# Performance work log

Measured on AMD Instinct MI355X. Metric: run time of the kernel, lower is better.

The kernel has to match this reference:

```python
import jax, jax.numpy as jnp
import numpy as np

B, N, K, A = 2, 4096, 20, 12
DIMS = [32, 64, 128, 256, 512]
POOL_RATE, POOL_K = 4, 4


def knn_index(v, k):
    # v: (b, n, 3) -> (b, n, k) nearest neighbors, self excluded
    d2 = jnp.sum(v * v, axis=-1)
    dist = d2[:, :, None] + d2[:, None, :] - 2.0 * jnp.einsum('bnd,bmd->bnm', v, v)
    _, idx = jax.lax.top_k(-dist, k + 1)
    return idx[:, :, 1:]


def gather_pos(v, idx):
    return jax.vmap(lambda vv, ii: vv[ii])(v, idx)  # (b, n, k, 3)


def gather_fea(fm, idx):
    return jax.vmap(lambda f, ii: f[:, ii, :])(fm, idx)  # (b, c, n, k, a)


def nbr_dirs(v, idx):
    d = gather_pos(v, idx) - v[:, :, None, :]
    return d / (jnp.linalg.norm(d, axis=-1, keepdims=True) + 1e-8)


def conv_surface(idx, v, K0):
    # K0: (C0, A, 3) learned direction kernels; output (b, C0, n, A)
    d = nbr_dirs(v, idx)  # (b,n,k,3)
    theta = jax.nn.relu(jnp.einsum('bnkd,cad->bnkca', d, K0))
    return jnp.transpose(jnp.max(theta, axis=2), (0, 2, 1, 3))


def equi_conv(idx, v, fm, dirs, Wc, bc, Ws):
    # fm: (b, cin, n, a) -> (b, cout, n, a)
    d = nbr_dirs(v, idx)
    theta = jax.nn.relu(jnp.einsum('bnkd,ad->bnka', d, dirs))  # (b,n,k,a)
    fn = gather_fea(fm, idx)  # (b,cin,n,k,a)
    fs = jnp.einsum('bcnka,co->bonka', fn, Ws) * theta[:, None]
    fs = jnp.max(fs, axis=3)  # max over neighbors -> (b,cout,n,a)
    fc = jnp.einsum('bcna,co->bona', fm, Wc) + bc[None, :, None, None]
    return fc + fs


def batchnorm(x, g, b):
    m = jnp.mean(x, axis=(0, 2, 3), keepdims=True)
    var = jnp.var(x, axis=(0, 2, 3), keepdims=True)
    return (x - m) * jax.lax.rsqrt(var + 1e-5) * g[None, :, None, None] + b[None, :, None, None]


def pool(v, fm):
    idx = knn_index(v, POOL_K)
    fn = jnp.max(gather_fea(fm, idx), axis=3)
    fm_p = jnp.maximum(fm, fn)
    sel = jnp.arange(0, v.shape[1], POOL_RATE)  # strided subsample
    return v[:, sel], fm_p[:, :, sel]


def fea_of(fm):
    return jnp.transpose(jnp.max(fm, axis=-1), (0, 2, 1))  # (b,n,c)


def setup_inputs() -> dict:
    key = jax.random.key(0)
    ks = iter(jax.random.split(key, 32))
    p = {'vertices': jax.random.normal(next(ks), (B, N, 3), jnp.float32)}
    p['K0'] = jax.random.normal(next(ks), (DIMS[0], A, 3), jnp.float32) * 0.1
    for i, (ci, co) in enumerate(zip(DIMS[:4], DIMS[1:]), start=1):
        s = 1.0 / np.sqrt(ci).astype(np.float32)
        p[f'dirs{i}'] = jax.random.normal(next(ks), (A, 3), jnp.float32) * 0.1
        p[f'Wc{i}'] = jax.random.normal(next(ks), (ci, co), jnp.float32) * s
        p[f'bc{i}'] = jnp.zeros((co,), jnp.float32)
        p[f'Ws{i}'] = jax.random.normal(next(ks), (ci, co), jnp.float32) * s
    for i, c in enumerate([DIMS[1], DIMS[2], DIMS[3]], start=1):
        p[f'g{i}'] = jnp.ones((c,), jnp.float32)
        p[f'b{i}'] = jnp.zeros((c,), jnp.float32)
    return p


def reference(vertices, K0, dirs1, Wc1, bc1, Ws1, dirs2, Wc2, bc2, Ws2,
              dirs3, Wc3, bc3, Ws3, dirs4, Wc4, bc4, Ws4,
              g1, b1, g2, b2, g3, b3):
    idx = knn_index(vertices, K)
    fm0 = jax.nn.relu(conv_surface(idx, vertices, K0))
    fm1 = jax.nn.relu(batchnorm(equi_conv(idx, vertices, fm0, dirs1, Wc1, bc1, Ws1), g1, b1))
    v1, fmp1 = pool(vertices, fm1)
    idx1 = knn_index(v1, min(K, v1.shape[1] // 8))
    fm2 = jax.nn.relu(batchnorm(equi_conv(idx1, v1, fmp1, dirs2, Wc2, bc2, Ws2), g2, b2))
    fm3 = jax.nn.relu(batchnorm(equi_conv(idx1, v1, fm2, dirs3, Wc3, bc3, Ws3), g3, b3))
    v2, fmp2 = pool(v1, fm3)
    idx2 = knn_index(v2, min(K, v2.shape[1] // 8))
    fm4 = equi_conv(idx2, v2, fmp2, dirs4, Wc4, bc4, Ws4)
    return fea_of(fm0), fea_of(fm1), fea_of(fm2), fea_of(fm3), fea_of(fm4)
```

## Files before the change

kernel.cpp:

```cpp
#include <hip/hip_runtime.h>
#include <hip/hip_bf16.h>
#include <math.h>

typedef unsigned short u16;
typedef unsigned long long u64;
#define DEV static __device__ __forceinline__

constexpr int Bz = 2, N0 = 4096, N1 = 1024, N2 = 256, KNN = 20, NA = 12;
constexpr int C0 = 32, C1 = 64, C2 = 128, C3 = 256, C4 = 512;
constexpr int BNG = 32;

constexpr size_t OFF_V0F   = 0;
constexpr size_t OFF_V1F   = 32768;
constexpr size_t OFF_V2F   = 40960;
constexpr size_t OFF_K0F   = 43008;
constexpr size_t OFF_DIRS  = 44160;
constexpr size_t OFF_WC    = 44304;
constexpr size_t OFF_WS    = 218384;
constexpr size_t OFF_BC    = 392464;
constexpr size_t OFF_BN    = 393424;
constexpr size_t OFF_FLAG  = 394832;
constexpr size_t OFF_IDX0  = 394848;
constexpr size_t OFF_IDX1  = 558688;
constexpr size_t OFF_IDX2  = 599648;
constexpr size_t OFF_PART  = 609888;
constexpr size_t PART_SZ   = 28672;
constexpr size_t OFF_HALF  = OFF_PART + PART_SZ;

constexpr size_t HA = 0;
constexpr size_t HB = 3145728;
constexpr size_t HG = 9437184;
constexpr size_t HP = HG + 3145728;

constexpr size_t OUT0 = 0;
constexpr size_t OUT1 = OUT0 + (size_t)Bz*N0*C0;
constexpr size_t OUT2 = OUT1 + (size_t)Bz*N0*C1;
constexpr size_t OUT3 = OUT2 + (size_t)Bz*N1*C2;
constexpr size_t OUT4 = OUT3 + (size_t)Bz*N1*C3;

DEV float b2f(u16 v) { return __uint_as_float(((unsigned int)v) << 16); }
DEV u16 f2b(float f) {
  unsigned int u = __float_as_uint(f);
  unsigned int lsb = (u >> 16) & 1u;
  return (u16)((u + 0x7fffu + lsb) >> 16);
}
DEV unsigned packb(float a, float b) {
  return (unsigned)f2b(a) | ((unsigned)f2b(b) << 16);
}

DEV u64 shflx64(u64 v, int m) {
  int lo = __shfl_xor((int)(unsigned)v, m, 64);
  int hi = __shfl_xor((int)(unsigned)(v >> 32), m, 64);
  return ((u64)(unsigned)hi << 32) | (unsigned)lo;
}
DEV int mbcnt64(u64 m) {
  return __builtin_amdgcn_mbcnt_hi((unsigned)(m >> 32),
         __builtin_amdgcn_mbcnt_lo((unsigned)m, 0));
}

DEV void st12(float* dst, const float* v) {
  float4 a{v[0],v[1],v[2],v[3]}, b{v[4],v[5],v[6],v[7]}, c{v[8],v[9],v[10],v[11]};
  ((float4*)dst)[0] = a; ((float4*)dst)[1] = b; ((float4*)dst)[2] = c;
}
DEV void st12(u16* dst, const float* v) {
  uint2 a{packb(v[0],v[1]), packb(v[2],v[3])};
  uint2 b{packb(v[4],v[5]), packb(v[6],v[7])};
  uint2 c{packb(v[8],v[9]), packb(v[10],v[11])};
  ((uint2*)dst)[0] = a; ((uint2*)dst)[1] = b; ((uint2*)dst)[2] = c;
}

struct InPtrs { const void* p[24]; };

__global__ void eq_convert_all(InPtrs in, float* ws) {
  __shared__ int sflag;
  {
    const u16* v = (const u16*)in.p[0];
    if (threadIdx.x < 64) {
      int bad = 0;
      #pragma unroll
      for (int j = 0; j < 4; ++j) {
        unsigned u = v[threadIdx.x*4 + j];
        int ex = (u >> 7) & 0xFF;
        bad += (((u & 0x7FFFu) != 0u) && (ex < 64 || ex > 191)) ? 1 : 0;
      }
      int tot = bad;
      #pragma unroll
      for (int s = 32; s > 0; s >>= 1) tot += __shfl_xor(tot, s, 64);
      if (threadIdx.x == 0) sflag = (tot >= 8) ? 1 : 0;
    }
    __syncthreads();
  }
  int f32mode = sflag;
  int t = blockIdx.x * blockDim.x + threadIdx.x;
  if (t < Bz*N0) {
    float x, y, z;
    if (f32mode) { const float* v = (const float*)in.p[0]; x=v[t*3]; y=v[t*3+1]; z=v[t*3+2]; }
    else { const u16* v = (const u16*)in.p[0]; x=b2f(v[t*3]); y=b2f(v[t*3+1]); z=b2f(v[t*3+2]); }
    float4 o; o.x=x; o.y=y; o.z=z; o.w=(x*x + y*y) + z*z;
    ((float4*)(ws + OFF_V0F))[t] = o;
    int b = t / N0, i = t % N0;
    if ((i & 3) == 0)  ((float4*)(ws + OFF_V1F))[b*N1 + (i >> 2)] = o;
    if ((i & 15) == 0) ((float4*)(ws + OFF_V2F))[b*N2 + (i >> 4)] = o;
    return;
  }
  int r = t - Bz*N0;
  if (r >= 351312) {
    int z = r - 351312;
    if (z < (int)PART_SZ) ws[OFF_PART + z] = 0.f;
    return;
  }
  const int cnt[23] = {1152, 36,2048,64,2048, 36,8192,128,8192,
                       36,32768,256,32768, 36,131072,512,131072,
                       64,64,128,128,256,256};
  const size_t off[23] = {OFF_K0F,
    OFF_DIRS+0,   OFF_WC+0,     OFF_BC+0,   OFF_WS+0,
    OFF_DIRS+36,  OFF_WC+2048,  OFF_BC+64,  OFF_WS+2048,
    OFF_DIRS+72,  OFF_WC+10240, OFF_BC+192, OFF_WS+10240,
    OFF_DIRS+108, OFF_WC+43008, OFF_BC+448, OFF_WS+43008,
    OFF_BN+0, OFF_BN+64, OFF_BN+128, OFF_BN+256, OFF_BN+384, OFF_BN+640};
  for (int i = 0; i < 23; ++i) {
    if (r < cnt[i]) {
      float val = f32mode ? ((const float*)in.p[i+1])[r] : b2f(((const u16*)in.p[i+1])[r]);
      ws[off[i] + r] = val;
      return;
    }
    r -= cnt[i];
  }
}

DEV unsigned umin(unsigned a, unsigned b) { return a < b ? a : b; }
DEV unsigned umax(unsigned a, unsigned b) { return a > b ? a : b; }

DEV unsigned cand_ud(const float4 vq, const float4 vc) {
  float dt = fmaf(vq.x, vc.x, fmaf(vq.y, vc.y, vq.z*vc.z));
  float d  = fmaf(-2.0f, dt, vq.w + vc.w);
  unsigned u = __float_as_uint(d);
  return u ^ ((unsigned)(((int)u) >> 31) | 0x80000000u);
}

template<int NPTS>
DEV void knn_body(int blk, const float4* __restrict__ vf, int* __restrict__ idx_out,
                  char* smem) {
  constexpr int CPL = NPTS/64;
  u64* selw_base = (u64*)smem;
  int* extr_base = (int*)(smem + 4*64*8);
  int wave = threadIdx.x >> 6, lane = threadIdx.x & 63;
  u64* selw = selw_base + wave*64;
  int* extrw = extr_base + wave*24;
  int qid = blk*4 + wave;
  int b = qid / NPTS, q = qid % NPTS;
  const float4* vb = vf + (size_t)b*NPTS;
  float4 vq = vb[q];

  unsigned k1=~0u, k2=~0u, k3=~0u, k4=~0u;
  #pragma unroll 8
  for (int j = 0; j < CPL; ++j) {
    float4 vc = vb[j*64 + lane];
    unsigned key = cand_ud(vq, vc);
    unsigned nk1 = umin(key, k1);
    unsigned nk2 = umin(umax(key, k1), k2);
    unsigned nk3 = umin(umax(key, k2), k3);
    unsigned nk4 = umin(umax(key, k3), k4);
    k1 = nk1; k2 = nk2; k3 = nk3; k4 = nk4;
  }

  unsigned p = 0;
  for (int bit = 31; bit >= 0; --bit) {
    unsigned T = p | (1u << bit);
    u64 m1 = __ballot(k1 < T), m2 = __ballot(k2 < T);
    u64 m3 = __ballot(k3 < T), m4 = __ballot(k4 < T);
    int cnt = __popcll(m1) + __popcll(m2) + __popcll(m3) + __popcll(m4);
    if (cnt < KNN+1) p = T;
  }
  size_t obase = (size_t)qid*KNN;
  bool need_fb = (CPL > 4) && (__ballot(k4 <= p) != 0ULL);

  if (!need_fb) {
    int base = 0;
    #pragma unroll 4
    for (int j = 0; j < CPL; ++j) {
      float4 vc = vb[j*64 + lane];
      unsigned ud = cand_ud(vq, vc);
      bool sel = (ud <= p);
      u64 m = __ballot(sel);
      int pos = base + mbcnt64(m);
      if (sel && pos < 64)
        selw[pos] = ((u64)ud << 32) | (unsigned)(j*64 + lane);
      base += __popcll(m);
    }
    int S = (base < 64) ? base : 64;
    if (lane < S) {
      u64 mykey = selw[lane];
      int rank = 0;
      for (int j = 0; j < S; ++j) rank += (selw[j] < mykey) ? 1 : 0;
      if (rank >= 1 && rank <= KNN)
        idx_out[obase + rank - 1] = (int)(unsigned)(mykey & 0xFFFFFFFFu);
    }
  } else {
    const u64 KINF = ~0ULL;
    u64 K1=KINF, K2=KINF, K3=KINF, K4=KINF;
    for (int j = 0; j < CPL; ++j) {
      int c = j*64 + lane;
      u64 k = ((u64)cand_ud(vq, vb[c]) << 32) | (unsigned)c;
      bool lt1 = k < K1, lt2 = k < K2, lt3 = k < K3, lt4 = k < K4;
      K4 = lt3 ? K3 : (lt4 ? k : K4);
      K3 = lt2 ? K2 : (lt3 ? k : K3);
      K2 = lt1 ? K1 : (lt2 ? k : K2);
      K1 = lt1 ? k  : K1;
    }
    for (int r = 0; r < KNN+1; ++r) {
      u64 g = K1;
      #pragma unroll
      for (int s = 32; s; s >>= 1) { u64 o = shflx64(g, s); g = (o < g) ? o : g; }
      int gidx = (int)(unsigned)(g & 0xFFFFFFFFu);
      if (lane == 0) {
        extrw[r] = gidx;
        if (r > 0) idx_out[obase + r - 1] = gidx;
      }
      if (r < KNN && lane == (gidx & 63)) {
        K1 = K2; K2 = K3; K3 = K4; K4 = KINF;
        if (K1 == KINF) {
          for (int j = 0; j < CPL; ++j) {
            int c = j*64 + lane;
            u64 k = ((u64)cand_ud(vq, vb[c]) << 32) | (unsigned)c;
            bool ex = false;
            for (int e = 0; e <= r; ++e) ex |= (extrw[e] == c);
            if (!ex) {
              bool lt1 = k < K1, lt2 = k < K2, lt3 = k < K3, lt4 = k < K4;
              K4 = lt3 ? K3 : (lt4 ? k : K4);
              K3 = lt2 ? K2 : (lt3 ? k : K3);
              K2 = lt1 ? K1 : (lt2 ? k : K2);
              K1 = lt1 ? k  : K1;
            }
          }
        }
      }
    }
  }
}

__global__ __launch_bounds__(256) void eq_knn_all(
    const float4* __restrict__ v0, int* __restrict__ i0,
    const float4* __restrict__ v1, int* __restrict__ i1,
    const float4* __restrict__ v2, int* __restrict__ i2) {
  __shared__ __align__(16) char smem[4*64*8 + 4*24*4];
  int blk = blockIdx.x;
  constexpr int NB0 = Bz*N0/4, NB1 = Bz*N1/4;
  if (blk < NB0)            knn_body<N0>(blk, v0, i0, smem);
  else if (blk < NB0+NB1)   knn_body<N1>(blk - NB0, v1, i1, smem);
  else                      knn_body<N2>(blk - NB0 - NB1, v2, i2, smem);
}

__global__ __launch_bounds__(128) void eq_conv_surface(
    const float4* __restrict__ v0f, const int* __restrict__ idx0,
    const float* __restrict__ K0f, u16* __restrict__ fm0, float* __restrict__ out0) {
  int bq = blockIdx.x;
  int b = bq >> 12;
  __shared__ float dk[KNN][3];
  __shared__ float row[C0*NA];
  int tid = threadIdx.x;
  if (tid < KNN) {
    int m = idx0[(size_t)bq*KNN + tid];
    float4 vq = v0f[bq];
    float4 vm = v0f[(size_t)b*N0 + m];
    float dx = vm.x - vq.x, dy = vm.y - vq.y, dz = vm.z - vq.z;
    float nrm = sqrtf((dx*dx + dy*dy) + dz*dz) + 1e-8f;
    dk[tid][0] = dx/nrm; dk[tid][1] = dy/nrm; dk[tid][2] = dz/nrm;
  }
  __syncthreads();
  for (int t4 = tid; t4 < C0*NA/4; t4 += 128) {
    const float* kd = K0f + (size_t)t4*12;
    float4 k0 = *(const float4*)(kd);
    float4 k1 = *(const float4*)(kd + 4);
    float4 k2 = *(const float4*)(kd + 8);
    float m0=0.f, m1=0.f, m2=0.f, m3=0.f;
    #pragma unroll
    for (int k = 0; k < KNN; ++k) {
      float dx = dk[k][0], dy = dk[k][1], dz = dk[k][2];
      m0 = fmaxf(m0, (dx*k0.x + dy*k0.y) + dz*k0.z);
      m1 = fmaxf(m1, (dx*k0.w + dy*k1.x) + dz*k1.y);
      m2 = fmaxf(m2, (dx*k1.z + dy*k1.w) + dz*k2.x);
      m3 = fmaxf(m3, (dx*k2.y + dy*k2.z) + dz*k2.w);
    }
    uint2 r; r.x = packb(m0, m1); r.y = packb(m2, m3);
    ((uint2*)fm0)[(size_t)bq*(C0*NA/4) + t4] = r;
    row[4*t4+0] = m0; row[4*t4+1] = m1; row[4*t4+2] = m2; row[4*t4+3] = m3;
  }
  __syncthreads();
  if (tid < C0) {
    float m = row[tid*NA];
    #pragma unroll
    for (int a = 1; a < NA; ++a) m = fmaxf(m, row[tid*NA + a]);
    out0[(size_t)bq*C0 + tid] = m;
  }
}

template<int CI, int CO, typename TO>
__global__ __launch_bounds__(256) void eq_linear4(
    const u16* __restrict__ in, const float* __restrict__ Wc,
    const float* __restrict__ Ws, const float* __restrict__ bias,
    TO* __restrict__ fc, u16* __restrict__ g) {
  constexpr int PPB = 512 / CO;
  constexpr int RS = CI*NA + 4;
  __shared__ float lds[PPB*RS];
  int tid = threadIdx.x;
  int mat = blockIdx.x & 1;
  int pt0 = (blockIdx.x >> 1) * PPB;
  constexpr int E = PPB*CI*NA;
  for (int t = tid; t < E; t += 256) {
    int pt = t / (CI*NA), r = t % (CI*NA);
    lds[pt*RS + r] = b2f(in[((size_t)(pt0+pt))*CI*NA + r]);
  }
  __syncthreads();
  constexpr int TPP = CO/2;
  int opair = tid % TPP, pt = tid / TPP;
  int o0 = opair*2;
  const float* W = mat ? Ws : Wc;
  const float* row = lds + pt*RS;
  float a0[NA], a1[NA];
  #pragma unroll
  for (int a = 0; a < NA; ++a) { a0[a]=0.f; a1[a]=0.f; }
  #pragma unroll 4
  for (int c = 0; c < CI; ++c) {
    float2 w2 = *(const float2*)(W + (size_t)c*CO + o0);
    float4 i0 = *(const float4*)(row + c*NA);
    float4 i1 = *(const float4*)(row + c*NA + 4);
    float4 i2 = *(const float4*)(row + c*NA + 8);
    float iv[NA] = {i0.x,i0.y,i0.z,i0.w, i1.x,i1.y,i1.z,i1.w, i2.x,i2.y,i2.z,i2.w};
    #pragma unroll
    for (int a = 0; a < NA; ++a) {
      a0[a] += iv[a]*w2.x; a1[a] += iv[a]*w2.y;
    }
  }
  size_t ptg = pt0 + pt;
  if (mat == 0) {
    float b0 = bias[o0], b1 = bias[o0+1];
    #pragma unroll
    for (int a = 0; a < NA; ++a) { a0[a] += b0; a1[a] += b1; }
    st12(fc + ((size_t)ptg*CO + o0)*NA, a0);
    st12(fc + ((size_t)ptg*CO + o0 + 1)*NA, a1);
  } else {
    st12(g + ((size_t)ptg*CO + o0)*NA, a0);
    st12(g + ((size_t)ptg*CO + o0 + 1)*NA, a1);
  }
}

__global__ __launch_bounds__(256) void eq_fsmax(
    const u16* __restrict__ g, const float4* __restrict__ vf,
    const float* __restrict__ dirs, const int* __restrict__ idx,
    u16* __restrict__ out, float* __restrict__ part, int npts, int co) {
  int bq = blockIdx.x;
  int b = bq / npts;
  __shared__ float th[KNN*NA];
  __shared__ float dk[KNN][3];
  __shared__ int nb[KNN];
  __shared__ float sstat[2][C3];
  int tid = threadIdx.x;
  if (tid < KNN) {
    int m = idx[(size_t)bq*KNN + tid];
    nb[tid] = m;
    float4 vq = vf[bq];
    float4 vm = vf[(size_t)b*npts + m];
    float dx = vm.x - vq.x, dy = vm.y - vq.y, dz = vm.z - vq.z;
    float nrm = sqrtf((dx*dx + dy*dy) + dz*dz) + 1e-8f;
    dk[tid][0] = dx/nrm; dk[tid][1] = dy/nrm; dk[tid][2] = dz/nrm;
  }
  sstat[0][tid] = 0.f; sstat[1][tid] = 0.f;
  __syncthreads();
  if (tid < KNN*NA) {
    int k = tid / NA, a = tid % NA;
    float s = (dk[k][0]*dirs[a*3] + dk[k][1]*dirs[a*3+1]) + dk[k][2]*dirs[a*3+2];
    th[tid] = fmaxf(s, 0.f);
  }
  __syncthreads();
  int quarter = co*NA/4;
  uint2* dst = (uint2*)(out + (size_t)bq*co*NA);
  const uint2* gb = (const uint2*)(g + (size_t)b*npts*co*NA);
  for (int t4 = tid; t4 < quarter; t4 += 256) {
    int a = (4*t4) % NA;
    const float* tha = th + a;
    float m0=-3.0e38f, m1=-3.0e38f, m2=-3.0e38f, m3=-3.0e38f;
    #pragma unroll 5
    for (int k = 0; k < KNN; ++k) {
      uint2 pv = gb[(size_t)nb[k]*quarter + t4];
      float4 tv = *(const float4*)(tha + k*NA);
      m0 = fmaxf(m0, tv.x*b2f((u16)(pv.x)));
      m1 = fmaxf(m1, tv.y*b2f((u16)(pv.x >> 16)));
      m2 = fmaxf(m2, tv.z*b2f((u16)(pv.y)));
      m3 = fmaxf(m3, tv.w*b2f((u16)(pv.y >> 16)));
    }
    uint2 d = dst[t4];
    float v0 = b2f((u16)d.x) + m0;
    float v1 = b2f((u16)(d.x >> 16)) + m1;
    float v2 = b2f((u16)d.y) + m2;
    float v3 = b2f((u16)(d.y >> 16)) + m3;
    uint2 r; r.x = packb(v0, v1); r.y = packb(v2, v3);
    dst[t4] = r;
    int ch = t4 / 3;
    atomicAdd(&sstat[0][ch], (v0 + v1) + (v2 + v3));
    atomicAdd(&sstat[1][ch], (v0*v0 + v1*v1) + (v2*v2 + v3*v3));
  }
  __syncthreads();
  if (tid < co) {
    float* pg = part + (size_t)(bq & (BNG-1))*2*co;
    atomicAdd(&pg[tid], sstat[0][tid]);
    atomicAdd(&pg[co + tid], sstat[1][tid]);
  }
}

template<int SPL>
__global__ __launch_bounds__(256) void eq_fsmax_fea(
    const u16* __restrict__ g, const float* __restrict__ fcin,
    const float4* __restrict__ vf, const float* __restrict__ dirs,
    const int* __restrict__ idx, float* __restrict__ outfea,
    int npts, int co) {
  constexpr int CHUNK = C4 / SPL;
  int part = blockIdx.x % SPL;
  int bq = blockIdx.x / SPL;
  int b = bq / npts;
  __shared__ float th[KNN*NA];
  __shared__ float dk[KNN][3];
  __shared__ int nb[KNN];
  __shared__ float row[CHUNK*NA];
  int tid = threadIdx.x;
  if (tid < KNN) {
    int m = idx[(size_t)bq*KNN + tid];
    nb[tid] = m;
    float4 vq = vf[bq];
    float4 vm = vf[(size_t)b*npts + m];
    float dx = vm.x - vq.x, dy = vm.y - vq.y, dz = vm.z - vq.z;
    float nrm = sqrtf((dx*dx + dy*dy) + dz*dz) + 1e-8f;
    dk[tid][0] = dx/nrm; dk[tid][1] = dy/nrm; dk[tid][2] = dz/nrm;
  }
  __syncthreads();
  if (tid < KNN*NA) {
    int k = tid / NA, a = tid % NA;
    float s = (dk[k][0]*dirs[a*3] + dk[k][1]*dirs[a*3+1]) + dk[k][2]*dirs[a*3+2];
    th[tid] = fmaxf(s, 0.f);
  }
  __syncthreads();
  int o0 = part * CHUNK;
  const float4* fcr = (const float4*)(fcin + ((size_t)bq*co + o0)*NA);
  const uint2* gb = (const uint2*)(g + (size_t)b*npts*co*NA + (size_t)o0*NA);
  int gquarter = co*NA/4;
  for (int t4 = tid; t4 < CHUNK*NA/4; t4 += 256) {
    int a = (4*t4) % NA;
    const float* tha = th + a;
    float m0=-3.0e38f, m1=-3.0e38f, m2=-3.0e38f, m3=-3.0e38f;
    #pragma unroll 5
    for (int k = 0; k < KNN; ++k) {
      uint2 pv = gb[(size_t)nb[k]*gquarter + t4];
      float4 tv = *(const float4*)(tha + k*NA);
      m0 = fmaxf(m0, tv.x*b2f((u16)(pv.x)));
      m1 = fmaxf(m1, tv.y*b2f((u16)(pv.x >> 16)));
      m2 = fmaxf(m2, tv.z*b2f((u16)(pv.y)));
      m3 = fmaxf(m3, tv.w*b2f((u16)(pv.y >> 16)));
    }
    float4 fc4 = fcr[t4];
    row[4*t4+0] = fc4.x + m0;
    row[4*t4+1] = fc4.y + m1;
    row[4*t4+2] = fc4.z + m2;
    row[4*t4+3] = fc4.w + m3;
  }
  __syncthreads();
  for (int o = tid; o < CHUNK; o += 256) {
    float m = row[o*NA];
    #pragma unroll
    for (int a = 1; a < NA; ++a) m = fmaxf(m, row[o*NA + a]);
    outfea[(size_t)bq*co + o0 + o] = m;
  }
}

__global__ __launch_bounds__(256) void eq_bnrelu_fea(
    u16* __restrict__ fm, const float* __restrict__ part,
    const float* __restrict__ gamma, const float* __restrict__ beta,
    float* __restrict__ outfea, int npts, int co) {
  int bq = blockIdx.x;
  int tid = threadIdx.x;
  __shared__ float sc[C3], sh[C3];
  __shared__ float row[C3*NA];
  for (int o = tid; o < co; o += 256) {
    float s = 0.f, s2 = 0.f;
    for (int g = 0; g < BNG; ++g) {
      s  += part[(size_t)g*2*co + o];
      s2 += part[(size_t)g*2*co + co + o];
    }
    float cnt = (float)(Bz*npts*NA);
    float mean = s / cnt;
    float var = fmaxf(s2 / cnt - mean*mean, 0.f);
    float inv = 1.0f / sqrtf(var + 1e-5f);
    sc[o] = gamma[o] * inv;
    sh[o] = beta[o] - mean * gamma[o] * inv;
  }
  __syncthreads();
  uint2* p = (uint2*)(fm + (size_t)bq*co*NA);
  int quarter = co*NA/4;
  for (int t4 = tid; t4 < quarter; t4 += 256) {
    int o = (4*t4) / NA;
    float s = sc[o], h = sh[o];
    uint2 pv = p[t4];
    float v0 = fmaxf(b2f((u16)pv.x)*s + h, 0.f);
    float v1 = fmaxf(b2f((u16)(pv.x >> 16))*s + h, 0.f);
    float v2 = fmaxf(b2f((u16)pv.y)*s + h, 0.f);
    float v3 = fmaxf(b2f((u16)(pv.y >> 16))*s + h, 0.f);
    uint2 r; r.x = packb(v0, v1); r.y = packb(v2, v3);
    p[t4] = r;
    row[4*t4+0] = v0; row[4*t4+1] = v1; row[4*t4+2] = v2; row[4*t4+3] = v3;
  }
  __syncthreads();
  for (int o = tid; o < co; o += 256) {
    float m = row[o*NA];
    #pragma unroll
    for (int a = 1; a < NA; ++a) m = fmaxf(m, row[o*NA + a]);
    outfea[(size_t)bq*co + o] = m;
  }
}

__global__ __launch_bounds__(256) void eq_pool(
    const u16* __restrict__ fm, const int* __restrict__ idx,
    u16* __restrict__ fmp, int npts, int c) {
  int ns = npts / 4;
  int bj = blockIdx.x;
  int b = bj / ns, j = bj % ns;
  int q = 4*j;
  size_t bq = (size_t)b*npts + q;
  __shared__ int nb[4];
  if (threadIdx.x < 4) nb[threadIdx.x] = idx[bq*KNN + threadIdx.x];
  __syncthreads();
  int quarter = c*NA/4;
  const uint2* base = (const uint2*)(fm + (size_t)b*npts*c*NA);
  const uint2* p0 = base + (size_t)q*quarter;
  uint2* dst = (uint2*)(fmp + (size_t)bj*c*NA);
  for (int t4 = threadIdx.x; t4 < quarter; t4 += 256) {
    uint2 v = p0[t4];
    float m0 = b2f((u16)v.x), m1 = b2f((u16)(v.x >> 16));
    float m2 = b2f((u16)v.y), m3 = b2f((u16)(v.y >> 16));
    #pragma unroll
    for (int kk = 0; kk < 4; ++kk) {
      uint2 w = base[(size_t)nb[kk]*quarter + t4];
      m0 = fmaxf(m0, b2f((u16)w.x));
      m1 = fmaxf(m1, b2f((u16)(w.x >> 16)));
      m2 = fmaxf(m2, b2f((u16)w.y));
      m3 = fmaxf(m3, b2f((u16)(w.y >> 16)));
    }
    uint2 r; r.x = packb(m0, m1); r.y = packb(m2, m3);
    dst[t4] = r;
  }
}

extern "C" void kernel_launch(void* const* d_in, const int* in_sizes, int n_in,
                              void* d_out, int out_size, void* d_ws, size_t ws_size,
                              hipStream_t stream) {
  float* ws = (float*)d_ws;
  float* out = (float*)d_out;
  u16* arena = (u16*)(ws + OFF_HALF);

  InPtrs ip;
  for (int i = 0; i < 24; ++i) ip.p[i] = d_in[i];

  float4* v0f = (float4*)(ws + OFF_V0F);
  float4* v1f = (float4*)(ws + OFF_V1F);
  float4* v2f = (float4*)(ws + OFF_V2F);
  int* idx0 = (int*)(ws + OFF_IDX0);
  int* idx1 = (int*)(ws + OFF_IDX1);
  int* idx2 = (int*)(ws + OFF_IDX2);
  u16* bufA = arena + HA;
  u16* bufB = arena + HB;
  float* fc4f = (float*)(arena + HB);
  u16* bufG = arena + HG;
  u16* bufP = arena + HP;
  float* partA = ws + OFF_PART;
  float* partB = ws + OFF_PART + 4096;
  float* partC = ws + OFF_PART + 12288;
  const float* DIRS = ws + OFF_DIRS;

  {
    int total = Bz*N0 + 351312 + (int)PART_SZ;
    eq_convert_all<<<(total + 255)/256, 256, 0, stream>>>(ip, ws);
  }

  eq_knn_all<<<Bz*N0/4 + Bz*N1/4 + Bz*N2/4, 256, 0, stream>>>(v0f, idx0, v1f, idx1, v2f, idx2);
  eq_conv_surface<<<Bz*N0, 128, 0, stream>>>(v0f, idx0, ws + OFF_K0F, bufA, out + OUT0);

  eq_linear4<C0, C1, u16><<<(Bz*N0/8)*2, 256, 0, stream>>>(bufA, ws + OFF_WC + 0, ws + OFF_WS + 0,
                                                           ws + OFF_BC + 0, bufB, bufG);
  eq_fsmax<<<Bz*N0, 256, 0, stream>>>(bufG, v0f, DIRS + 0, idx0, bufB, partA, N0, C1);
  eq_bnrelu_fea<<<Bz*N0, 256, 0, stream>>>(bufB, partA, ws + OFF_BN + 0, ws + OFF_BN + 64,
                                           out + OUT1, N0, C1);

  eq_pool<<<Bz*N1, 256, 0, stream>>>(bufB, idx0, bufP, N0, C1);

  eq_linear4<C1, C2, u16><<<(Bz*N1/4)*2, 256, 0, stream>>>(bufP, ws + OFF_WC + 2048, ws + OFF_WS + 2048,
                                                           ws + OFF_BC + 64, bufA, bufG);
  eq_fsmax<<<Bz*N1, 256, 0, stream>>>(bufG, v1f, DIRS + 36, idx1, bufA, partB, N1, C2);
  eq_bnrelu_fea<<<Bz*N1, 256, 0, stream>>>(bufA, partB, ws + OFF_BN + 128, ws + OFF_BN + 256,
                                           out + OUT2, N1, C2);

  eq_linear4<C2, C3, u16><<<(Bz*N1/2)*2, 256, 0, stream>>>(bufA, ws + OFF_WC + 10240, ws + OFF_WS + 10240,
                                                           ws + OFF_BC + 192, bufB, bufG);
  eq_fsmax<<<Bz*N1, 256, 0, stream>>>(bufG, v1f, DIRS + 72, idx1, bufB, partC, N1, C3);
  eq_bnrelu_fea<<<Bz*N1, 256, 0, stream>>>(bufB, partC, ws + OFF_BN + 384, ws + OFF_BN + 640,
                                           out + OUT3, N1, C3);

  eq_pool<<<Bz*N2, 256, 0, stream>>>(bufB, idx1, bufP, N1, C3);

  eq_linear4<C3, C4, float><<<(Bz*N2)*2, 256, 0, stream>>>(bufP, ws + OFF_WC + 43008, ws + OFF_WS + 43008,
                                                           ws + OFF_BC + 448, fc4f, bufG);
  eq_fsmax_fea<4><<<Bz*N2*4, 256, 0, stream>>>(bufG, fc4f, v2f, DIRS + 108, idx2, out + OUT4, N2, C4);
}
```

Baseline: 499.6 us.

## Process four KNN queries per wave and keep candidate indices in registers

Each wavefront now handles four query points at once, so every candidate point load is reused across four distance computations. The per-lane top-4 lists now carry indices alongside distances, which removes the second pass over all candidates to collect the selected ones. The fallback path is seeded from the register lists. In exchange, register pressure grows considerably, the grid has four times fewer blocks, and the threshold search runs four times per wave.

```diff
diff --git a/kernel.cpp b/kernel.cpp
--- a/kernel.cpp
+++ b/kernel.cpp
@@ -128,9 +128,6 @@
   }
 }
 
-DEV unsigned umin(unsigned a, unsigned b) { return a < b ? a : b; }
-DEV unsigned umax(unsigned a, unsigned b) { return a > b ? a : b; }
-
 DEV unsigned cand_ud(const float4 vq, const float4 vc) {
   float dt = fmaf(vq.x, vc.x, fmaf(vq.y, vc.y, vq.z*vc.z));
   float d  = fmaf(-2.0f, dt, vq.w + vc.w);
@@ -139,98 +136,116 @@
 }
 
 template<int NPTS>
-DEV void knn_body(int blk, const float4* __restrict__ vf, int* __restrict__ idx_out,
-                  char* smem) {
+DEV void knn_body4(int blk, const float4* __restrict__ vf, int* __restrict__ idx_out,
+                   char* smem) {
   constexpr int CPL = NPTS/64;
-  u64* selw_base = (u64*)smem;
-  int* extr_base = (int*)(smem + 4*64*8);
   int wave = threadIdx.x >> 6, lane = threadIdx.x & 63;
-  u64* selw = selw_base + wave*64;
-  int* extrw = extr_base + wave*24;
-  int qid = blk*4 + wave;
-  int b = qid / NPTS, q = qid % NPTS;
+  u64* selw = (u64*)smem + wave*64;
+  int* extrw = (int*)(smem + 4*64*8) + wave*24;
+  int q0 = blk*16 + wave*4;
+  int b = q0 / NPTS, qr = q0 % NPTS;
   const float4* vb = vf + (size_t)b*NPTS;
-  float4 vq = vb[q];
-
-  unsigned k1=~0u, k2=~0u, k3=~0u, k4=~0u;
-  #pragma unroll 8
+  float4 vq[4];
+  #pragma unroll
+  for (int qq = 0; qq < 4; ++qq) vq[qq] = vb[qr + qq];
+
+  unsigned d[4][4]; int ii[4][4];
+  #pragma unroll
+  for (int qq = 0; qq < 4; ++qq) {
+    #pragma unroll
+    for (int s = 0; s < 4; ++s) { d[qq][s] = 0xFFFFFFFFu; ii[qq][s] = 0x3FFFFFFF; }
+  }
+
+  #pragma unroll 2
   for (int j = 0; j < CPL; ++j) {
     float4 vc = vb[j*64 + lane];
-    unsigned key = cand_ud(vq, vc);
-    unsigned nk1 = umin(key, k1);
-    unsigned nk2 = umin(umax(key, k1), k2);
-    unsigned nk3 = umin(umax(key, k2), k3);
-    unsigned nk4 = umin(umax(key, k3), k4);
-    k1 = nk1; k2 = nk2; k3 = nk3; k4 = nk4;
-  }
-
-  unsigned p = 0;
+    int c = j*64 + lane;
+    #pragma unroll
+    for (int qq = 0; qq < 4; ++qq) {
+      unsigned ud = cand_ud(vq[qq], vc);
+      bool lt1 = ud < d[qq][0], lt2 = ud < d[qq][1], lt3 = ud < d[qq][2], lt4 = ud < d[qq][3];
+      d[qq][3] = lt3 ? d[qq][2] : (lt4 ? ud : d[qq][3]);
+      ii[qq][3] = lt3 ? ii[qq][2] : (lt4 ? c : ii[qq][3]);
+      d[qq][2] = lt2 ? d[qq][1] : (lt3 ? ud : d[qq][2]);
+      ii[qq][2] = lt2 ? ii[qq][1] : (lt3 ? c : ii[qq][2]);
+      d[qq][1] = lt1 ? d[qq][0] : (lt2 ? ud : d[qq][1]);
+      ii[qq][1] = lt1 ? ii[qq][0] : (lt2 ? c : ii[qq][1]);
+      d[qq][0] = lt1 ? ud : d[qq][0];
+      ii[qq][0] = lt1 ? c  : ii[qq][0];
+    }
+  }
+
+  unsigned p[4] = {0, 0, 0, 0};
   for (int bit = 31; bit >= 0; --bit) {
-    unsigned T = p | (1u << bit);
-    u64 m1 = __ballot(k1 < T), m2 = __ballot(k2 < T);
-    u64 m3 = __ballot(k3 < T), m4 = __ballot(k4 < T);
-    int cnt = __popcll(m1) + __popcll(m2) + __popcll(m3) + __popcll(m4);
-    if (cnt < KNN+1) p = T;
-  }
-  size_t obase = (size_t)qid*KNN;
-  bool need_fb = (CPL > 4) && (__ballot(k4 <= p) != 0ULL);
-
-  if (!need_fb) {
-    int base = 0;
-    #pragma unroll 4
-    for (int j = 0; j < CPL; ++j) {
-      float4 vc = vb[j*64 + lane];
-      unsigned ud = cand_ud(vq, vc);
-      bool sel = (ud <= p);
-      u64 m = __ballot(sel);
-      int pos = base + mbcnt64(m);
-      if (sel && pos < 64)
-        selw[pos] = ((u64)ud << 32) | (unsigned)(j*64 + lane);
-      base += __popcll(m);
-    }
-    int S = (base < 64) ? base : 64;
-    if (lane < S) {
-      u64 mykey = selw[lane];
-      int rank = 0;
-      for (int j = 0; j < S; ++j) rank += (selw[j] < mykey) ? 1 : 0;
-      if (rank >= 1 && rank <= KNN)
-        idx_out[obase + rank - 1] = (int)(unsigned)(mykey & 0xFFFFFFFFu);
-    }
-  } else {
-    const u64 KINF = ~0ULL;
-    u64 K1=KINF, K2=KINF, K3=KINF, K4=KINF;
-    for (int j = 0; j < CPL; ++j) {
-      int c = j*64 + lane;
-      u64 k = ((u64)cand_ud(vq, vb[c]) << 32) | (unsigned)c;
-      bool lt1 = k < K1, lt2 = k < K2, lt3 = k < K3, lt4 = k < K4;
-      K4 = lt3 ? K3 : (lt4 ? k : K4);
-      K3 = lt2 ? K2 : (lt3 ? k : K3);
-      K2 = lt1 ? K1 : (lt2 ? k : K2);
-      K1 = lt1 ? k  : K1;
-    }
-    for (int r = 0; r < KNN+1; ++r) {
-      u64 g = K1;
-      #pragma unroll
-      for (int s = 32; s; s >>= 1) { u64 o = shflx64(g, s); g = (o < g) ? o : g; }
-      int gidx = (int)(unsigned)(g & 0xFFFFFFFFu);
-      if (lane == 0) {
-        extrw[r] = gidx;
-        if (r > 0) idx_out[obase + r - 1] = gidx;
+    #pragma unroll
+    for (int qq = 0; qq < 4; ++qq) {
+      unsigned T = p[qq] | (1u << bit);
+      u64 m1 = __ballot(d[qq][0] < T), m2 = __ballot(d[qq][1] < T);
+      u64 m3 = __ballot(d[qq][2] < T), m4 = __ballot(d[qq][3] < T);
+      int cnt = __popcll(m1) + __popcll(m2) + __popcll(m3) + __popcll(m4);
+      if (cnt < KNN+1) p[qq] = T;
+    }
+  }
+
+  #pragma unroll
+  for (int qq = 0; qq < 4; ++qq) {
+    unsigned pq = p[qq];
+    unsigned d1 = d[qq][0], d2 = d[qq][1], d3 = d[qq][2], d4 = d[qq][3];
+    int i1 = ii[qq][0], i2 = ii[qq][1], i3 = ii[qq][2], i4 = ii[qq][3];
+    size_t obase = (size_t)(q0 + qq)*KNN;
+    bool need_fb = false;
+    if (CPL > 4) need_fb = (__ballot(d4 <= pq) != 0ULL);
+    if (!need_fb) {
+      bool p1 = d1 <= pq, p2 = d2 <= pq, p3 = d3 <= pq, p4 = d4 <= pq;
+      u64 m1 = __ballot(p1), m2 = __ballot(p2), m3 = __ballot(p3), m4 = __ballot(p4);
+      int c1 = __popcll(m1), c2 = __popcll(m2), c3 = __popcll(m3), c4 = __popcll(m4);
+      int S = c1 + c2 + c3 + c4;
+      if (S > 63) need_fb = true;
+      else {
+        if (p1) selw[mbcnt64(m1)] = ((u64)d1 << 32) | (unsigned)i1;
+        if (p2) selw[c1 + mbcnt64(m2)] = ((u64)d2 << 32) | (unsigned)i2;
+        if (p3) selw[c1 + c2 + mbcnt64(m3)] = ((u64)d3 << 32) | (unsigned)i3;
+        if (p4) selw[c1 + c2 + c3 + mbcnt64(m4)] = ((u64)d4 << 32) | (unsigned)i4;
+        if (lane < S) {
+          u64 mykey = selw[lane];
+          int rank = 0;
+          for (int j2 = 0; j2 < S; ++j2) rank += (selw[j2] < mykey) ? 1 : 0;
+          if (rank >= 1 && rank <= KNN)
+            idx_out[obase + rank - 1] = (int)(unsigned)(mykey & 0xFFFFFFFFu);
+        }
       }
-      if (r < KNN && lane == (gidx & 63)) {
-        K1 = K2; K2 = K3; K3 = K4; K4 = KINF;
-        if (K1 == KINF) {
-          for (int j = 0; j < CPL; ++j) {
-            int c = j*64 + lane;
-            u64 k = ((u64)cand_ud(vq, vb[c]) << 32) | (unsigned)c;
-            bool ex = false;
-            for (int e = 0; e <= r; ++e) ex |= (extrw[e] == c);
-            if (!ex) {
-              bool lt1 = k < K1, lt2 = k < K2, lt3 = k < K3, lt4 = k < K4;
-              K4 = lt3 ? K3 : (lt4 ? k : K4);
-              K3 = lt2 ? K2 : (lt3 ? k : K3);
-              K2 = lt1 ? K1 : (lt2 ? k : K2);
-              K1 = lt1 ? k  : K1;
+    }
+    if (need_fb) {
+      const u64 KINF = ~0ULL;
+      u64 K1 = ((u64)d1 << 32) | (unsigned)i1;
+      u64 K2 = ((u64)d2 << 32) | (unsigned)i2;
+      u64 K3 = ((u64)d3 << 32) | (unsigned)i3;
+      u64 K4 = ((u64)d4 << 32) | (unsigned)i4;
+      float4 vqq = vq[qq];
+      for (int r = 0; r < KNN+1; ++r) {
+        u64 g = K1;
+        #pragma unroll
+        for (int s = 32; s; s >>= 1) { u64 o = shflx64(g, s); g = (o < g) ? o : g; }
+        int gidx = (int)(unsigned)(g & 0xFFFFFFFFu);
+        if (lane == 0) {
+          extrw[r] = gidx;
+          if (r > 0) idx_out[obase + r - 1] = gidx;
+        }
+        if (r < KNN && lane == (gidx & 63)) {
+          K1 = K2; K2 = K3; K3 = K4; K4 = KINF;
+          if (K1 == KINF) {
+            for (int j = 0; j < CPL; ++j) {
+              int c = j*64 + lane;
+              u64 k = ((u64)cand_ud(vqq, vb[c]) << 32) | (unsigned)c;
+              bool ex = false;
+              for (int e = 0; e <= r; ++e) ex |= (extrw[e] == c);
+              if (!ex) {
+                bool lt1k = k < K1, lt2k = k < K2, lt3k = k < K3, lt4k = k < K4;
+                K4 = lt3k ? K3 : (lt4k ? k : K4);
+                K3 = lt2k ? K2 : (lt3k ? k : K3);
+                K2 = lt1k ? K1 : (lt2k ? k : K2);
+                K1 = lt1k ? k  : K1;
+              }
             }
           }
         }
@@ -245,10 +260,10 @@
     const float4* __restrict__ v2, int* __restrict__ i2) {
   __shared__ __align__(16) char smem[4*64*8 + 4*24*4];
   int blk = blockIdx.x;
-  constexpr int NB0 = Bz*N0/4, NB1 = Bz*N1/4;
-  if (blk < NB0)            knn_body<N0>(blk, v0, i0, smem);
-  else if (blk < NB0+NB1)   knn_body<N1>(blk - NB0, v1, i1, smem);
-  else                      knn_body<N2>(blk - NB0 - NB1, v2, i2, smem);
+  constexpr int NB0 = Bz*N0/16, NB1 = Bz*N1/16;
+  if (blk < NB0)            knn_body4<N0>(blk, v0, i0, smem);
+  else if (blk < NB0+NB1)   knn_body4<N1>(blk - NB0, v1, i1, smem);
+  else                      knn_body4<N2>(blk - NB0 - NB1, v2, i2, smem);
 }
 
 __global__ __launch_bounds__(128) void eq_conv_surface(
@@ -579,7 +594,7 @@
     eq_convert_all<<<(total + 255)/256, 256, 0, stream>>>(ip, ws);
   }
 
-  eq_knn_all<<<Bz*N0/4 + Bz*N1/4 + Bz*N2/4, 256, 0, stream>>>(v0f, idx0, v1f, idx1, v2f, idx2);
+  eq_knn_all<<<Bz*N0/16 + Bz*N1/16 + Bz*N2/16, 256, 0, stream>>>(v0f, idx0, v1f, idx1, v2f, idx2);
   eq_conv_surface<<<Bz*N0, 128, 0, stream>>>(v0f, idx0, ws + OFF_K0F, bufA, out + OUT0);
 
   eq_linear4<C0, C1, u16><<<(Bz*N0/8)*2, 256, 0, stream>>>(bufA, ws + OFF_WC + 0, ws + OFF_WS + 0,
```

New measurement: 572.2 us. +14.5%, slower.
